# Optimization experiments

Hardware: AMD Instinct MI355X
Metric: run time of the kernel (lower is better)

Reference implementation:

```python
import jax, jax.numpy as jnp
import numpy as np

B = 262144
Z_DIM = 128
H = 100


def setup_inputs() -> dict:
    key = jax.random.key(0)
    ks = jax.random.split(key, 7)
    x = jax.random.normal(ks[0], (B, Z_DIM), dtype=jnp.float32)
    # torch.nn.Linear default init ~ U(-1/sqrt(fan_in), 1/sqrt(fan_in)); use scaled normals
    w1 = jax.random.normal(ks[1], (H, Z_DIM), dtype=jnp.float32) / np.sqrt(Z_DIM)
    b1 = jax.random.normal(ks[2], (H,), dtype=jnp.float32) * 0.01
    w2 = jax.random.normal(ks[3], (H, H), dtype=jnp.float32) / np.sqrt(H)
    b2 = jax.random.normal(ks[4], (H,), dtype=jnp.float32) * 0.01
    w3 = jax.random.normal(ks[5], (9, H), dtype=jnp.float32) / np.sqrt(H)
    b3 = jax.random.normal(ks[6], (9,), dtype=jnp.float32) * 0.01
    return {"x": x, "w1": w1, "b1": b1, "w2": w2, "b2": b2, "w3": w3, "b3": b3}


def reference(x, w1, b1, w2, b2, w3, b3):
    h = jax.nn.relu(x @ w1.T + b1)            # [B, 100]
    h = jnp.tanh(h @ w2.T + b2)               # [B, 100]
    m = h @ w3.T + b3                         # [B, 9]
    M = m.reshape(-1, 3, 3)                   # [B, 3, 3]
    # torch.svd: M = U diag(S) V^T ; R_hat = U @ V^T == u @ vh (jax convention)
    u, s, vh = jnp.linalg.svd(M, full_matrices=False)
    R_hat = u @ vh                            # [B, 3, 3] nearest orthogonal (Procrustes)
    return R_hat.reshape(-1, 9)
```

## Files before the change

kernel.cpp:

```cpp
#include <hip/hip_runtime.h>
#include <math.h>

#define ZDIM 128
#define HDIM 100

__global__ void prep_transpose(const float* __restrict__ w1,
                               const float* __restrict__ w3,
                               float* __restrict__ w1t,
                               float* __restrict__ w3t) {
    int idx = blockIdx.x * blockDim.x + threadIdx.x;
    if (idx < HDIM * ZDIM) {
        int j = idx / ZDIM;
        int k = idx - j * ZDIM;
        w1t[k * HDIM + j] = w1[idx];
    }
    if (idx < 9 * HDIM) {
        int r = idx / HDIM;
        int i = idx - r * HDIM;
        w3t[i * 9 + r] = w3[idx];
    }
}

__device__ __forceinline__ float fast_tanh(float v) {
    float e = __expf(2.0f * v);
    return (e - 1.0f) / (e + 1.0f);
}

template<bool TR>
__global__ __launch_bounds__(256, 4) void pose_main(
    const float* __restrict__ x,
    const float* __restrict__ w1,
    const float* __restrict__ b1,
    const float* __restrict__ w2,
    const float* __restrict__ b2,
    const float* __restrict__ w3,
    const float* __restrict__ b3,
    const float* __restrict__ w1t,
    const float* __restrict__ w3t,
    float* __restrict__ out,
    int nB)
{
    int tid = blockIdx.x * blockDim.x + threadIdx.x;
    if (tid >= nB) return;

    const float4* xrow4 = reinterpret_cast<const float4*>(x + (size_t)tid * ZDIM);

    float h1[HDIM];
    #pragma unroll
    for (int j = 0; j < HDIM; ++j) h1[j] = b1[j];

    float4 cur = xrow4[0];
    #pragma unroll 1
    for (int k4 = 0; k4 < ZDIM / 4; ++k4) {
        float4 nxt = xrow4[(k4 + 1) & (ZDIM / 4 - 1)];
        const float xs[4] = { cur.x, cur.y, cur.z, cur.w };
        #pragma unroll
        for (int kk = 0; kk < 4; ++kk) {
            const int k = k4 * 4 + kk;
            const float xv = xs[kk];
            if (TR) {
                const float* wrow = w1t + (size_t)k * HDIM;
                #pragma unroll
                for (int j = 0; j < HDIM; ++j)
                    h1[j] = fmaf(xv, wrow[j], h1[j]);
            } else {
                #pragma unroll
                for (int j = 0; j < HDIM; ++j)
                    h1[j] = fmaf(xv, w1[(size_t)j * ZDIM + k], h1[j]);
            }
        }
        cur = nxt;
    }

    #pragma unroll
    for (int j = 0; j < HDIM; ++j) h1[j] = fmaxf(h1[j], 0.0f);

    float mr[9];
    #pragma unroll
    for (int r = 0; r < 9; ++r) mr[r] = b3[r];

    #pragma unroll 2
    for (int i = 0; i < HDIM; ++i) {
        const float* w2row = w2 + (size_t)i * HDIM;
        float a0 = 0.f, a1 = 0.f, a2 = 0.f, a3 = 0.f;
        #pragma unroll
        for (int j = 0; j < HDIM; j += 4) {
            a0 = fmaf(w2row[j + 0], h1[j + 0], a0);
            a1 = fmaf(w2row[j + 1], h1[j + 1], a1);
            a2 = fmaf(w2row[j + 2], h1[j + 2], a2);
            a3 = fmaf(w2row[j + 3], h1[j + 3], a3);
        }
        float t = fast_tanh((a0 + a1) + (a2 + a3) + b2[i]);
        #pragma unroll
        for (int r = 0; r < 9; ++r) {
            float wv = TR ? w3t[i * 9 + r] : w3[r * HDIM + i];
            mr[r] = fmaf(wv, t, mr[r]);
        }
    }

    double X00 = mr[0], X01 = mr[1], X02 = mr[2];
    double X10 = mr[3], X11 = mr[4], X12 = mr[5];
    double X20 = mr[6], X21 = mr[7], X22 = mr[8];

    #pragma unroll 1
    for (int it = 0; it < 10; ++it) {
        double C00 = X11 * X22 - X12 * X21;
        double C01 = X12 * X20 - X10 * X22;
        double C02 = X10 * X21 - X11 * X20;
        double C10 = X02 * X21 - X01 * X22;
        double C11 = X00 * X22 - X02 * X20;
        double C12 = X01 * X20 - X00 * X21;
        double C20 = X01 * X12 - X02 * X11;
        double C21 = X02 * X10 - X00 * X12;
        double C22 = X00 * X11 - X01 * X10;
        double det = X00 * C00 + X01 * C01 + X02 * C02;
        double adet = fabs(det);
        adet = adet < 1e-300 ? 1e-300 : adet;
        double sdet = (det < 0.0) ? -adet : adet;
        double nf2 = X00*X00 + X01*X01 + X02*X02
                   + X10*X10 + X11*X11 + X12*X12
                   + X20*X20 + X21*X21 + X22*X22;
        double nc2 = C00*C00 + C01*C01 + C02*C02
                   + C10*C10 + C11*C11 + C12*C12
                   + C20*C20 + C21*C21 + C22*C22;
        double g = sqrt(sqrt(nc2 / nf2) / adet);
        double a = 0.5 * g;
        double b = 0.5 / (g * sdet);
        X00 = a * X00 + b * C00;  X01 = a * X01 + b * C01;  X02 = a * X02 + b * C02;
        X10 = a * X10 + b * C10;  X11 = a * X11 + b * C11;  X12 = a * X12 + b * C12;
        X20 = a * X20 + b * C20;  X21 = a * X21 + b * C21;  X22 = a * X22 + b * C22;
    }

    float* o = out + (size_t)tid * 9;
    o[0] = (float)X00; o[1] = (float)X01; o[2] = (float)X02;
    o[3] = (float)X10; o[4] = (float)X11; o[5] = (float)X12;
    o[6] = (float)X20; o[7] = (float)X21; o[8] = (float)X22;
}

extern "C" void kernel_launch(void* const* d_in, const int* in_sizes, int n_in,
                              void* d_out, int out_size, void* d_ws, size_t ws_size,
                              hipStream_t stream) {
    const float* x  = (const float*)d_in[0];
    const float* w1 = (const float*)d_in[1];
    const float* b1 = (const float*)d_in[2];
    const float* w2 = (const float*)d_in[3];
    const float* b2 = (const float*)d_in[4];
    const float* w3 = (const float*)d_in[5];
    const float* b3 = (const float*)d_in[6];
    float* out = (float*)d_out;

    int nB = in_sizes[0] / ZDIM;

    const size_t need = (size_t)(HDIM * ZDIM + HDIM * 9) * sizeof(float);
    float* w1t = (float*)d_ws;
    float* w3t = w1t + HDIM * ZDIM;

    dim3 block(256);
    dim3 grid((nB + 255) / 256);

    if (ws_size >= need) {
        dim3 pgrid((HDIM * ZDIM + 255) / 256);
        prep_transpose<<<pgrid, block, 0, stream>>>(w1, w3, w1t, w3t);
        pose_main<true><<<grid, block, 0, stream>>>(x, w1, b1, w2, b2, w3, b3,
                                                    w1t, w3t, out, nB);
    } else {
        pose_main<false><<<grid, block, 0, stream>>>(x, w1, b1, w2, b2, w3, b3,
                                                     nullptr, nullptr, out, nB);
    }
}
```

Before: 208.1 us.

## Split each sample's MLP across two lanes with padded packed weights

Each sample is now handled by two adjacent threads, each computing half of the hidden layer (50 units, padded to 52) and combining the layer-2 dot products with a lane shuffle. Weights are prepacked into padded, float4-aligned layouts for vectorized uniform loads. Polar iterations drop from 10 to 8. This halves per-thread register arrays to improve occupancy, at the cost of duplicated x loads, duplicated layer-3 and polar work in both lanes, and slightly fewer refinement iterations.

Result: slower. 789.0 us (+279.1%).

```diff
diff --git a/kernel.cpp b/kernel.cpp
--- a/kernel.cpp
+++ b/kernel.cpp
@@ -3,21 +3,34 @@
 
 #define ZDIM 128
 #define HDIM 100
-
-__global__ void prep_transpose(const float* __restrict__ w1,
-                               const float* __restrict__ w3,
-                               float* __restrict__ w1t,
-                               float* __restrict__ w3t) {
+#define JP   52
+#define JP4  (JP / 4)
+
+__global__ void prep_pack(const float* __restrict__ w1,
+                          const float* __restrict__ w2,
+                          const float* __restrict__ w3,
+                          float* __restrict__ w1p,
+                          float* __restrict__ w2p,
+                          float* __restrict__ w3t) {
     int idx = blockIdx.x * blockDim.x + threadIdx.x;
-    if (idx < HDIM * ZDIM) {
-        int j = idx / ZDIM;
-        int k = idx - j * ZDIM;
-        w1t[k * HDIM + j] = w1[idx];
-    }
-    if (idx < 9 * HDIM) {
-        int r = idx / HDIM;
-        int i = idx - r * HDIM;
-        w3t[i * 9 + r] = w3[idx];
+    if (idx < ZDIM * 2 * JP) {
+        int k = idx / (2 * JP);
+        int r = idx - k * 2 * JP;
+        int h = r / JP;
+        int j = r - h * JP;
+        w1p[idx] = (j < 50) ? w1[(size_t)(h * 50 + j) * ZDIM + k] : 0.0f;
+    }
+    if (idx < HDIM * 2 * JP) {
+        int i = idx / (2 * JP);
+        int r = idx - i * 2 * JP;
+        int h = r / JP;
+        int j = r - h * JP;
+        w2p[idx] = (j < 50) ? w2[(size_t)i * HDIM + h * 50 + j] : 0.0f;
+    }
+    if (idx < HDIM * 9) {
+        int i = idx / 9;
+        int r = idx - i * 9;
+        w3t[idx] = w3[(size_t)r * HDIM + i];
     }
 }
 
@@ -26,28 +39,61 @@
     return (e - 1.0f) / (e + 1.0f);
 }
 
-template<bool TR>
-__global__ __launch_bounds__(256, 4) void pose_main(
+__device__ __forceinline__ void polar3x3(const float mr[9], double X[9]) {
+    #pragma unroll
+    for (int r = 0; r < 9; ++r) X[r] = (double)mr[r];
+    #pragma unroll 1
+    for (int it = 0; it < 8; ++it) {
+        double C00 = X[4]*X[8] - X[5]*X[7];
+        double C01 = X[5]*X[6] - X[3]*X[8];
+        double C02 = X[3]*X[7] - X[4]*X[6];
+        double C10 = X[2]*X[7] - X[1]*X[8];
+        double C11 = X[0]*X[8] - X[2]*X[6];
+        double C12 = X[1]*X[6] - X[0]*X[7];
+        double C20 = X[1]*X[5] - X[2]*X[4];
+        double C21 = X[2]*X[3] - X[0]*X[5];
+        double C22 = X[0]*X[4] - X[1]*X[3];
+        double det = X[0]*C00 + X[1]*C01 + X[2]*C02;
+        double adet = fabs(det);
+        adet = adet < 1e-300 ? 1e-300 : adet;
+        double sdet = (det < 0.0) ? -adet : adet;
+        double nf2 = X[0]*X[0]+X[1]*X[1]+X[2]*X[2]+X[3]*X[3]+X[4]*X[4]
+                   + X[5]*X[5]+X[6]*X[6]+X[7]*X[7]+X[8]*X[8];
+        double nc2 = C00*C00+C01*C01+C02*C02+C10*C10+C11*C11
+                   + C12*C12+C20*C20+C21*C21+C22*C22;
+        double g = sqrt(sqrt(nc2 / nf2) / adet);
+        double a = 0.5 * g;
+        double b = 0.5 / (g * sdet);
+        double Y0 = a*X[0] + b*C00, Y1 = a*X[1] + b*C01, Y2 = a*X[2] + b*C02;
+        double Y3 = a*X[3] + b*C10, Y4 = a*X[4] + b*C11, Y5 = a*X[5] + b*C12;
+        double Y6 = a*X[6] + b*C20, Y7 = a*X[7] + b*C21, Y8 = a*X[8] + b*C22;
+        X[0]=Y0; X[1]=Y1; X[2]=Y2; X[3]=Y3; X[4]=Y4; X[5]=Y5; X[6]=Y6; X[7]=Y7; X[8]=Y8;
+    }
+}
+
+__global__ __launch_bounds__(256) void pose_split(
     const float* __restrict__ x,
-    const float* __restrict__ w1,
     const float* __restrict__ b1,
-    const float* __restrict__ w2,
     const float* __restrict__ b2,
-    const float* __restrict__ w3,
     const float* __restrict__ b3,
-    const float* __restrict__ w1t,
+    const float* __restrict__ w1p,
+    const float* __restrict__ w2p,
     const float* __restrict__ w3t,
     float* __restrict__ out,
     int nB)
 {
     int tid = blockIdx.x * blockDim.x + threadIdx.x;
-    if (tid >= nB) return;
-
-    const float4* xrow4 = reinterpret_cast<const float4*>(x + (size_t)tid * ZDIM);
-
-    float h1[HDIM];
-    #pragma unroll
-    for (int j = 0; j < HDIM; ++j) h1[j] = b1[j];
+    int s = tid >> 1;
+    int h = tid & 1;
+    if (s >= nB) return;
+
+    const float4* xrow4 = reinterpret_cast<const float4*>(x + (size_t)s * ZDIM);
+    const float4* w1p4 = reinterpret_cast<const float4*>(w1p) + (size_t)h * JP4;
+    const float4* w2p4 = reinterpret_cast<const float4*>(w2p) + (size_t)h * JP4;
+
+    float acc[JP];
+    #pragma unroll
+    for (int j = 0; j < JP; ++j) acc[j] = (j < 50) ? b1[h * 50 + j] : 0.0f;
 
     float4 cur = xrow4[0];
     #pragma unroll 1
@@ -57,29 +103,87 @@
         #pragma unroll
         for (int kk = 0; kk < 4; ++kk) {
             const int k = k4 * 4 + kk;
+            const float4* wr = w1p4 + (size_t)k * (2 * JP4);
             const float xv = xs[kk];
-            if (TR) {
-                const float* wrow = w1t + (size_t)k * HDIM;
-                #pragma unroll
-                for (int j = 0; j < HDIM; ++j)
-                    h1[j] = fmaf(xv, wrow[j], h1[j]);
-            } else {
-                #pragma unroll
-                for (int j = 0; j < HDIM; ++j)
-                    h1[j] = fmaf(xv, w1[(size_t)j * ZDIM + k], h1[j]);
+            #pragma unroll
+            for (int j4 = 0; j4 < JP4; ++j4) {
+                float4 w = wr[j4];
+                acc[4*j4+0] = fmaf(xv, w.x, acc[4*j4+0]);
+                acc[4*j4+1] = fmaf(xv, w.y, acc[4*j4+1]);
+                acc[4*j4+2] = fmaf(xv, w.z, acc[4*j4+2]);
+                acc[4*j4+3] = fmaf(xv, w.w, acc[4*j4+3]);
             }
         }
         cur = nxt;
     }
-
+    #pragma unroll
+    for (int j = 0; j < JP; ++j) acc[j] = fmaxf(acc[j], 0.0f);
+
+    float mr[9];
+    #pragma unroll
+    for (int r = 0; r < 9; ++r) mr[r] = b3[r];
+
+    #pragma unroll 2
+    for (int i = 0; i < HDIM; ++i) {
+        const float4* wr = w2p4 + (size_t)i * (2 * JP4);
+        float a0 = 0.f, a1 = 0.f, a2 = 0.f, a3 = 0.f;
+        #pragma unroll
+        for (int j4 = 0; j4 < JP4; ++j4) {
+            float4 w = wr[j4];
+            a0 = fmaf(w.x, acc[4*j4+0], a0);
+            a1 = fmaf(w.y, acc[4*j4+1], a1);
+            a2 = fmaf(w.z, acc[4*j4+2], a2);
+            a3 = fmaf(w.w, acc[4*j4+3], a3);
+        }
+        float part = (a0 + a1) + (a2 + a3);
+        float full = part + __shfl_xor(part, 1);
+        float t = fast_tanh(full + b2[i]);
+        #pragma unroll
+        for (int r = 0; r < 9; ++r)
+            mr[r] = fmaf(w3t[i * 9 + r], t, mr[r]);
+    }
+
+    double X[9];
+    polar3x3(mr, X);
+
+    float* o = out + (size_t)s * 9;
+    if (h == 0) {
+        o[0] = (float)X[0]; o[1] = (float)X[1]; o[2] = (float)X[2];
+        o[3] = (float)X[3]; o[4] = (float)X[4];
+    } else {
+        o[5] = (float)X[5]; o[6] = (float)X[6];
+        o[7] = (float)X[7]; o[8] = (float)X[8];
+    }
+}
+
+__global__ __launch_bounds__(256) void pose_simple(
+    const float* __restrict__ x,
+    const float* __restrict__ w1, const float* __restrict__ b1,
+    const float* __restrict__ w2, const float* __restrict__ b2,
+    const float* __restrict__ w3, const float* __restrict__ b3,
+    float* __restrict__ out, int nB)
+{
+    int tid = blockIdx.x * blockDim.x + threadIdx.x;
+    if (tid >= nB) return;
+    const float* xrow = x + (size_t)tid * ZDIM;
+
+    float h1[HDIM];
+    #pragma unroll
+    for (int j = 0; j < HDIM; ++j) h1[j] = b1[j];
+    #pragma unroll 1
+    for (int k = 0; k < ZDIM; ++k) {
+        float xv = xrow[k];
+        #pragma unroll
+        for (int j = 0; j < HDIM; ++j)
+            h1[j] = fmaf(xv, w1[(size_t)j * ZDIM + k], h1[j]);
+    }
     #pragma unroll
     for (int j = 0; j < HDIM; ++j) h1[j] = fmaxf(h1[j], 0.0f);
 
     float mr[9];
     #pragma unroll
     for (int r = 0; r < 9; ++r) mr[r] = b3[r];
-
-    #pragma unroll 2
+    #pragma unroll 1
     for (int i = 0; i < HDIM; ++i) {
         const float* w2row = w2 + (size_t)i * HDIM;
         float a0 = 0.f, a1 = 0.f, a2 = 0.f, a3 = 0.f;
@@ -92,49 +196,15 @@
         }
         float t = fast_tanh((a0 + a1) + (a2 + a3) + b2[i]);
         #pragma unroll
-        for (int r = 0; r < 9; ++r) {
-            float wv = TR ? w3t[i * 9 + r] : w3[r * HDIM + i];
-            mr[r] = fmaf(wv, t, mr[r]);
-        }
-    }
-
-    double X00 = mr[0], X01 = mr[1], X02 = mr[2];
-    double X10 = mr[3], X11 = mr[4], X12 = mr[5];
-    double X20 = mr[6], X21 = mr[7], X22 = mr[8];
-
-    #pragma unroll 1
-    for (int it = 0; it < 10; ++it) {
-        double C00 = X11 * X22 - X12 * X21;
-        double C01 = X12 * X20 - X10 * X22;
-        double C02 = X10 * X21 - X11 * X20;
-        double C10 = X02 * X21 - X01 * X22;
-        double C11 = X00 * X22 - X02 * X20;
-        double C12 = X01 * X20 - X00 * X21;
-        double C20 = X01 * X12 - X02 * X11;
-        double C21 = X02 * X10 - X00 * X12;
-        double C22 = X00 * X11 - X01 * X10;
-        double det = X00 * C00 + X01 * C01 + X02 * C02;
-        double adet = fabs(det);
-        adet = adet < 1e-300 ? 1e-300 : adet;
-        double sdet = (det < 0.0) ? -adet : adet;
-        double nf2 = X00*X00 + X01*X01 + X02*X02
-                   + X10*X10 + X11*X11 + X12*X12
-                   + X20*X20 + X21*X21 + X22*X22;
-        double nc2 = C00*C00 + C01*C01 + C02*C02
-                   + C10*C10 + C11*C11 + C12*C12
-                   + C20*C20 + C21*C21 + C22*C22;
-        double g = sqrt(sqrt(nc2 / nf2) / adet);
-        double a = 0.5 * g;
-        double b = 0.5 / (g * sdet);
-        X00 = a * X00 + b * C00;  X01 = a * X01 + b * C01;  X02 = a * X02 + b * C02;
-        X10 = a * X10 + b * C10;  X11 = a * X11 + b * C11;  X12 = a * X12 + b * C12;
-        X20 = a * X20 + b * C20;  X21 = a * X21 + b * C21;  X22 = a * X22 + b * C22;
-    }
-
+        for (int r = 0; r < 9; ++r)
+            mr[r] = fmaf(w3[(size_t)r * HDIM + i], t, mr[r]);
+    }
+
+    double X[9];
+    polar3x3(mr, X);
     float* o = out + (size_t)tid * 9;
-    o[0] = (float)X00; o[1] = (float)X01; o[2] = (float)X02;
-    o[3] = (float)X10; o[4] = (float)X11; o[5] = (float)X12;
-    o[6] = (float)X20; o[7] = (float)X21; o[8] = (float)X22;
+    #pragma unroll
+    for (int r = 0; r < 9; ++r) o[r] = (float)X[r];
 }
 
 extern "C" void kernel_launch(void* const* d_in, const int* in_sizes, int n_in,
@@ -151,20 +221,24 @@
 
     int nB = in_sizes[0] / ZDIM;
 
-    const size_t need = (size_t)(HDIM * ZDIM + HDIM * 9) * sizeof(float);
-    float* w1t = (float*)d_ws;
-    float* w3t = w1t + HDIM * ZDIM;
-
-    dim3 block(256);
-    dim3 grid((nB + 255) / 256);
+    const size_t n_w1p = (size_t)ZDIM * 2 * JP;
+    const size_t n_w2p = (size_t)HDIM * 2 * JP;
+    const size_t n_w3t = (size_t)HDIM * 9;
+    const size_t need  = (n_w1p + n_w2p + n_w3t) * sizeof(float);
 
     if (ws_size >= need) {
-        dim3 pgrid((HDIM * ZDIM + 255) / 256);
-        prep_transpose<<<pgrid, block, 0, stream>>>(w1, w3, w1t, w3t);
-        pose_main<true><<<grid, block, 0, stream>>>(x, w1, b1, w2, b2, w3, b3,
-                                                    w1t, w3t, out, nB);
+        float* w1p = (float*)d_ws;
+        float* w2p = w1p + n_w1p;
+        float* w3t = w2p + n_w2p;
+
+        int prep_n = (int)n_w1p;
+        prep_pack<<<(prep_n + 255) / 256, 256, 0, stream>>>(w1, w2, w3, w1p, w2p, w3t);
+
+        long long threads = 2LL * nB;
+        dim3 grid((unsigned)((threads + 255) / 256));
+        pose_split<<<grid, 256, 0, stream>>>(x, b1, b2, b3, w1p, w2p, w3t, out, nB);
     } else {
-        pose_main<false><<<grid, block, 0, stream>>>(x, w1, b1, w2, b2, w3, b3,
-                                                     nullptr, nullptr, out, nB);
-    }
-}
+        dim3 grid((nB + 255) / 256);
+        pose_simple<<<grid, 256, 0, stream>>>(x, w1, b1, w2, b2, w3, b3, out, nB);
+    }
+}
```
